# Kernel optimization log

Hardware: AMD Instinct MI355X
Metric: run time of the kernel (lower is better)

The kernel has to match this reference:

```python
import jax, jax.numpy as jnp
import numpy as np

N_DIM = 3            # Cl(3,0) for 3D point clouds
ALG_DIM = 1 << N_DIM # 8 multivector components
SUBSPACE_REPS = np.array([1, 3, 3, 1])  # grade sizes 0..3
LN_EPS = 1e-5


def build_cayley(n=N_DIM, metric=(1.0, 1.0, 1.0)):
    """Cayley tensor C[i, j, k] = coeff of e_j in e_i * e_k, basis sorted by (grade, lex)."""
    dim = 1 << n
    masks = sorted(range(dim), key=lambda m: (bin(m).count('1'), m))
    idx = {m: i for i, m in enumerate(masks)}
    cay = np.zeros((dim, dim, dim), dtype=np.float32)
    for i, a in enumerate(masks):
        for k, b in enumerate(masks):
            swaps = 0
            t = a >> 1
            while t:
                swaps += bin(t & b).count('1')
                t >>= 1
            sign = -1.0 if (swaps & 1) else 1.0
            for bit in range(n):
                if (a & b) & (1 << bit):
                    sign *= metric[bit]
            cay[i, idx[a ^ b], k] = sign
    return cay


def setup_inputs() -> dict:
    key = jax.random.key(0)
    ks = jax.random.split(key, 5)
    B, S, D = 4, 1024, ALG_DIM
    return {
        'x': jax.random.normal(ks[0], (B, S, D), dtype=jnp.float32),
        'Wq': jax.random.normal(ks[1], (S, S, 4), dtype=jnp.float32) * 0.02,
        'bq': jax.random.normal(ks[2], (S,), dtype=jnp.float32) * 0.02,
        'Wk': jax.random.normal(ks[3], (S, S, 4), dtype=jnp.float32) * 0.02,
        'bk': jax.random.normal(ks[4], (S,), dtype=jnp.float32) * 0.02,
        'gamma': jnp.ones((D,), dtype=jnp.float32),
        'beta': jnp.zeros((D,), dtype=jnp.float32),
    }


def reference(x, Wq, bq, Wk, bk, gamma, beta):
    cayley = jnp.asarray(build_cayley(), dtype=jnp.float16)  # [8,8,8]

    def mvlinear(inp, W, b):
        # expand per-grade weights to per-component: [S,S,4] -> [S,S,8]
        Wf = jnp.repeat(W, SUBSPACE_REPS, axis=-1, total_repeat_length=ALG_DIM)
        out = jnp.einsum('bmi,nmi->bni', inp, Wf)  # mix along sequence axis
        return out.at[:, :, 0].add(b[None, :])      # bias on scalar component only

    def layernorm(h):
        mu = h.mean(-1, keepdims=True)
        var = ((h - mu) ** 2).mean(-1, keepdims=True)
        return (h - mu) / jnp.sqrt(var + LN_EPS) * gamma + beta

    q = layernorm(mvlinear(x, Wq, bq)).astype(jnp.float16)  # [B,S,8]
    k = layernorm(mvlinear(x, Wk, bk)).astype(jnp.float16)  # [B,S,8]
    # pairwise geometric product: out[b,n,m,j] = sum_ik q[b,n,i] C[i,j,k] k[b,m,k]
    out = jnp.einsum('bni,ijk,bmk->bnmj', q, cayley, k)
    return out.astype(jnp.float32)
```

## Files before the change

kernel.cpp:

```cpp
#include <hip/hip_runtime.h>
#include <hip/hip_fp16.h>

#define SEQ 1024
#define BATCH 4
#define GP_BLOCKS 2048

typedef float f32x4 __attribute__((ext_vector_type(4)));

struct InvTab { int qi[8][8]; int ki[8][8]; float s[8][8]; };

constexpr InvTab build_inv() {
  InvTab v{};
  int masks[8] = {0, 1, 2, 4, 3, 5, 6, 7};
  int idx[8]   = {0, 0, 0, 0, 0, 0, 0, 0};
  for (int p = 0; p < 8; ++p) idx[masks[p]] = p;
  int cnt[8] = {0, 0, 0, 0, 0, 0, 0, 0};
  for (int i = 0; i < 8; ++i) {
    for (int k = 0; k < 8; ++k) {
      int a = masks[i], bm = masks[k];
      int swaps = 0;
      int tt = a >> 1;
      while (tt) {
        int u = tt & bm;
        while (u) { swaps += u & 1; u >>= 1; }
        tt >>= 1;
      }
      int j = idx[a ^ bm];
      int c = cnt[j]++;
      v.qi[j][c] = i;
      v.ki[j][c] = k;
      v.s[j][c]  = (swaps & 1) ? -1.0f : 1.0f;
    }
  }
  return v;
}
constexpr InvTab INV = build_inv();

union H8 { float4 f4; __half h[8]; };

__global__ __launch_bounds__(256) void qk_kernel(
    const float* __restrict__ x,
    const float* __restrict__ Wq,
    const float* __restrict__ bq,
    const float* __restrict__ Wk,
    const float* __restrict__ bk,
    const float* __restrict__ gamma,
    const float* __restrict__ beta,
    __half* __restrict__ qout,
    __half* __restrict__ kout)
{
  __shared__ float4 lds[2048];

  const int n    = blockIdx.x;
  const int b    = threadIdx.x >> 6;
  const int lane = threadIdx.x & 63;

  {
    const float4* wq4 = (const float4*)(Wq + (size_t)n * SEQ * 4);
    const float4* wk4 = (const float4*)(Wk + (size_t)n * SEQ * 4);
#pragma unroll
    for (int t = 0; t < 4; ++t) {
      int idx = threadIdx.x + t * 256;
      lds[idx]        = wq4[idx];
      lds[1024 + idx] = wk4[idx];
    }
  }
  __syncthreads();

  const float* xb = x + (size_t)b * SEQ * 8;

  float aq[8], ak[8];
#pragma unroll
  for (int i = 0; i < 8; ++i) { aq[i] = 0.0f; ak[i] = 0.0f; }

  for (int m = lane; m < SEQ; m += 64) {
    float4 x0 = *(const float4*)(xb + (size_t)m * 8);
    float4 x1 = *(const float4*)(xb + (size_t)m * 8 + 4);
    float4 q4 = lds[m];
    float4 k4 = lds[1024 + m];

    aq[0] = fmaf(x0.x, q4.x, aq[0]);
    aq[1] = fmaf(x0.y, q4.y, aq[1]);
    aq[2] = fmaf(x0.z, q4.y, aq[2]);
    aq[3] = fmaf(x0.w, q4.y, aq[3]);
    aq[4] = fmaf(x1.x, q4.z, aq[4]);
    aq[5] = fmaf(x1.y, q4.z, aq[5]);
    aq[6] = fmaf(x1.z, q4.z, aq[6]);
    aq[7] = fmaf(x1.w, q4.w, aq[7]);

    ak[0] = fmaf(x0.x, k4.x, ak[0]);
    ak[1] = fmaf(x0.y, k4.y, ak[1]);
    ak[2] = fmaf(x0.z, k4.y, ak[2]);
    ak[3] = fmaf(x0.w, k4.y, ak[3]);
    ak[4] = fmaf(x1.x, k4.z, ak[4]);
    ak[5] = fmaf(x1.y, k4.z, ak[5]);
    ak[6] = fmaf(x1.z, k4.z, ak[6]);
    ak[7] = fmaf(x1.w, k4.w, ak[7]);
  }

  float v[8];
  const bool odd = (lane & 1) != 0;
#pragma unroll
  for (int i = 0; i < 8; ++i) {
    float tq = __shfl_xor(aq[i], 1, 64);
    float tk = __shfl_xor(ak[i], 1, 64);
    v[i] = odd ? (ak[i] + tk) : (aq[i] + tq);
  }
#pragma unroll
  for (int off = 2; off < 64; off <<= 1) {
#pragma unroll
    for (int i = 0; i < 8; ++i) v[i] += __shfl_xor(v[i], off, 64);
  }

  if (lane < 2) {
    v[0] += odd ? bk[n] : bq[n];

    float mu = 0.0f;
#pragma unroll
    for (int i = 0; i < 8; ++i) mu += v[i];
    mu *= 0.125f;
    float var = 0.0f;
#pragma unroll
    for (int i = 0; i < 8; ++i) { float d = v[i] - mu; var = fmaf(d, d, var); }
    var *= 0.125f;
    float inv = rsqrtf(var + 1e-5f);

    H8 u;
#pragma unroll
    for (int i = 0; i < 8; ++i)
      u.h[i] = __float2half((v[i] - mu) * inv * gamma[i] + beta[i]);

    __half* dst = odd ? kout : qout;
    *(float4*)(dst + ((size_t)b * SEQ + n) * 8) = u.f4;
  }
}

__global__ __launch_bounds__(256) void gp_kernel(
    const __half* __restrict__ q,
    const __half* __restrict__ k,
    float* __restrict__ out)
{
  const int wave = threadIdx.x >> 6;
  const int lane = threadIdx.x & 63;
  const int h    = lane >> 5;
  const int STRIDE = GP_BLOCKS * 128;
  const int POINTS = BATCH * SEQ * SEQ;

  int p = blockIdx.x * 128 + wave * 32 + (lane & 31);

#pragma unroll 1
  for (int it = 0; it < POINTS / STRIDE; ++it, p += STRIDE) {
    const int m  = p & (SEQ - 1);
    const int bn = p >> 10;
    const int b  = bn >> 10;

    H8 uq, uk;
    uq.f4 = *(const float4*)(q + (size_t)bn * 8);
    uk.f4 = *(const float4*)(k + ((size_t)b * SEQ + m) * 8);

    float qf[8], kf[8];
#pragma unroll
    for (int i = 0; i < 8; ++i) {
      qf[i] = __half2float(uq.h[i]);
      kf[i] = __half2float(uk.h[i]);
    }

    float o0 = 0.0f, o1 = 0.0f, o2 = 0.0f, o3 = 0.0f;
    if (h == 0) {
#pragma unroll
      for (int c = 0; c < 8; ++c) {
        o0 = fmaf(INV.s[0][c] * qf[INV.qi[0][c]], kf[INV.ki[0][c]], o0);
        o1 = fmaf(INV.s[1][c] * qf[INV.qi[1][c]], kf[INV.ki[1][c]], o1);
        o2 = fmaf(INV.s[2][c] * qf[INV.qi[2][c]], kf[INV.ki[2][c]], o2);
        o3 = fmaf(INV.s[3][c] * qf[INV.qi[3][c]], kf[INV.ki[3][c]], o3);
      }
    } else {
#pragma unroll
      for (int c = 0; c < 8; ++c) {
        o0 = fmaf(INV.s[4][c] * qf[INV.qi[4][c]], kf[INV.ki[4][c]], o0);
        o1 = fmaf(INV.s[5][c] * qf[INV.qi[5][c]], kf[INV.ki[5][c]], o1);
        o2 = fmaf(INV.s[6][c] * qf[INV.qi[6][c]], kf[INV.ki[6][c]], o2);
        o3 = fmaf(INV.s[7][c] * qf[INV.qi[7][c]], kf[INV.ki[7][c]], o3);
      }
    }

    f32x4 val = {o0, o1, o2, o3};
    __builtin_nontemporal_store(val, (f32x4*)(out + (size_t)p * 8 + h * 4));
  }
}

extern "C" void kernel_launch(void* const* d_in, const int* in_sizes, int n_in,
                              void* d_out, int out_size, void* d_ws, size_t ws_size,
                              hipStream_t stream) {
  const float* x     = (const float*)d_in[0];
  const float* Wq    = (const float*)d_in[1];
  const float* bq    = (const float*)d_in[2];
  const float* Wk    = (const float*)d_in[3];
  const float* bk    = (const float*)d_in[4];
  const float* gamma = (const float*)d_in[5];
  const float* beta  = (const float*)d_in[6];

  __half* qbuf = (__half*)d_ws;
  __half* kbuf = qbuf + (size_t)BATCH * SEQ * 8;

  qk_kernel<<<SEQ, 256, 0, stream>>>(x, Wq, bq, Wk, bk, gamma, beta, qbuf, kbuf);

  gp_kernel<<<GP_BLOCKS, 256, 0, stream>>>(qbuf, kbuf, (float*)d_out);
}
```

Measured before the change: 41.73 us.

## Split qk reduction across 512 threads and hoist q row per wave in gp

The qk kernel now runs 512 threads per block, splitting the sequence reduction into two halves per batch and combining the partials through shared memory before the layernorm. This doubles the parallelism available to hide load latency. The gp kernel now gives each wave half of one output row, so the q vector is loaded and converted once per wave and only k is loaded per iteration, with simpler index arithmetic. The cost is an extra LDS reduction and barrier in qk, and a fixed mapping of work to waves in gp.

```diff
diff --git a/kernel.cpp b/kernel.cpp
--- a/kernel.cpp
+++ b/kernel.cpp
@@ -38,7 +38,7 @@
 
 union H8 { float4 f4; __half h[8]; };
 
-__global__ __launch_bounds__(256) void qk_kernel(
+__global__ __launch_bounds__(512) void qk_kernel(
     const float* __restrict__ x,
     const float* __restrict__ Wq,
     const float* __restrict__ bq,
@@ -50,17 +50,20 @@
     __half* __restrict__ kout)
 {
   __shared__ float4 lds[2048];
-
-  const int n    = blockIdx.x;
-  const int b    = threadIdx.x >> 6;
-  const int lane = threadIdx.x & 63;
+  __shared__ float red[8][2][8];
+
+  const int n     = blockIdx.x;
+  const int w     = threadIdx.x >> 6;
+  const int lane  = threadIdx.x & 63;
+  const int b     = w & 3;
+  const int mhalf = w >> 2;
 
   {
     const float4* wq4 = (const float4*)(Wq + (size_t)n * SEQ * 4);
     const float4* wk4 = (const float4*)(Wk + (size_t)n * SEQ * 4);
 #pragma unroll
-    for (int t = 0; t < 4; ++t) {
-      int idx = threadIdx.x + t * 256;
+    for (int t = 0; t < 2; ++t) {
+      int idx = threadIdx.x + t * 512;
       lds[idx]        = wq4[idx];
       lds[1024 + idx] = wk4[idx];
     }
@@ -73,7 +76,9 @@
 #pragma unroll
   for (int i = 0; i < 8; ++i) { aq[i] = 0.0f; ak[i] = 0.0f; }
 
-  for (int m = lane; m < SEQ; m += 64) {
+#pragma unroll
+  for (int it = 0; it < 8; ++it) {
+    int m = mhalf * 512 + it * 64 + lane;
     float4 x0 = *(const float4*)(xb + (size_t)m * 8);
     float4 x1 = *(const float4*)(xb + (size_t)m * 8 + 4);
     float4 q4 = lds[m];
@@ -113,25 +118,39 @@
   }
 
   if (lane < 2) {
-    v[0] += odd ? bk[n] : bq[n];
+#pragma unroll
+    for (int i = 0; i < 8; ++i) red[w][lane][i] = v[i];
+  }
+  __syncthreads();
+
+  if (threadIdx.x < 8) {
+    const int t  = threadIdx.x;
+    const int qk = t >> 2;
+    const int bb = t & 3;
+
+    float s[8];
+#pragma unroll
+    for (int i = 0; i < 8; ++i) s[i] = red[bb][qk][i] + red[4 + bb][qk][i];
+
+    s[0] += qk ? bk[n] : bq[n];
 
     float mu = 0.0f;
 #pragma unroll
-    for (int i = 0; i < 8; ++i) mu += v[i];
+    for (int i = 0; i < 8; ++i) mu += s[i];
     mu *= 0.125f;
     float var = 0.0f;
 #pragma unroll
-    for (int i = 0; i < 8; ++i) { float d = v[i] - mu; var = fmaf(d, d, var); }
+    for (int i = 0; i < 8; ++i) { float d = s[i] - mu; var = fmaf(d, d, var); }
     var *= 0.125f;
     float inv = rsqrtf(var + 1e-5f);
 
     H8 u;
 #pragma unroll
     for (int i = 0; i < 8; ++i)
-      u.h[i] = __float2half((v[i] - mu) * inv * gamma[i] + beta[i]);
-
-    __half* dst = odd ? kout : qout;
-    *(float4*)(dst + ((size_t)b * SEQ + n) * 8) = u.f4;
+      u.h[i] = __float2half((s[i] - mu) * inv * gamma[i] + beta[i]);
+
+    __half* dst = qk ? kout : qout;
+    *(float4*)(dst + ((size_t)bb * SEQ + n) * 8) = u.f4;
   }
 }
 
@@ -143,27 +162,29 @@
   const int wave = threadIdx.x >> 6;
   const int lane = threadIdx.x & 63;
   const int h    = lane >> 5;
-  const int STRIDE = GP_BLOCKS * 128;
-  const int POINTS = BATCH * SEQ * SEQ;
-
-  int p = blockIdx.x * 128 + wave * 32 + (lane & 31);
+  const int W    = blockIdx.x * 4 + wave;
+  const int bn   = W >> 1;
+  const int b    = bn >> 10;
+  const int mb   = (W & 1) * 512;
+
+  H8 uq;
+  uq.f4 = *(const float4*)(q + (size_t)bn * 8);
+  float qf[8];
+#pragma unroll
+  for (int i = 0; i < 8; ++i) qf[i] = __half2float(uq.h[i]);
+
+  const __half* krow = k + (size_t)b * SEQ * 8;
+  float* orow = out + ((size_t)bn * SEQ + mb) * 8;
 
 #pragma unroll 1
-  for (int it = 0; it < POINTS / STRIDE; ++it, p += STRIDE) {
-    const int m  = p & (SEQ - 1);
-    const int bn = p >> 10;
-    const int b  = bn >> 10;
-
-    H8 uq, uk;
-    uq.f4 = *(const float4*)(q + (size_t)bn * 8);
-    uk.f4 = *(const float4*)(k + ((size_t)b * SEQ + m) * 8);
-
-    float qf[8], kf[8];
-#pragma unroll
-    for (int i = 0; i < 8; ++i) {
-      qf[i] = __half2float(uq.h[i]);
-      kf[i] = __half2float(uk.h[i]);
-    }
+  for (int it = 0; it < 16; ++it) {
+    const int mo = it * 32 + (lane & 31);
+
+    H8 uk;
+    uk.f4 = *(const float4*)(krow + (size_t)(mb + mo) * 8);
+    float kf[8];
+#pragma unroll
+    for (int i = 0; i < 8; ++i) kf[i] = __half2float(uk.h[i]);
 
     float o0 = 0.0f, o1 = 0.0f, o2 = 0.0f, o3 = 0.0f;
     if (h == 0) {
@@ -185,7 +206,7 @@
     }
 
     f32x4 val = {o0, o1, o2, o3};
-    __builtin_nontemporal_store(val, (f32x4*)(out + (size_t)p * 8 + h * 4));
+    __builtin_nontemporal_store(val, (f32x4*)(orow + (size_t)mo * 8 + h * 4));
   }
 }
 
@@ -203,7 +224,7 @@
   __half* qbuf = (__half*)d_ws;
   __half* kbuf = qbuf + (size_t)BATCH * SEQ * 8;
 
-  qk_kernel<<<SEQ, 256, 0, stream>>>(x, Wq, bq, Wk, bk, gamma, beta, qbuf, kbuf);
+  qk_kernel<<<SEQ, 512, 0, stream>>>(x, Wq, bq, Wk, bk, gamma, beta, qbuf, kbuf);
 
   gp_kernel<<<GP_BLOCKS, 256, 0, stream>>>(qbuf, kbuf, (float*)d_out);
 }
```

New measurement: 44.30 us. +6.2%, slower.
